# Kernel tuning notes

Measured on AMD Instinct MI355X. Metric: run time of the kernel, lower is better.

Reference implementation:

```python
import jax, jax.numpy as jnp
import numpy as np

EMBED_DIM = 2048
N_HEADS = 32
N_GROUPS = 8
HEAD_SIZE = EMBED_DIM // N_HEADS  # 64
SCALE = HEAD_SIZE ** -0.5
B, S = 2, 2048


def setup_inputs() -> dict:
    key = jax.random.key(0)
    ks = jax.random.split(key, 7)
    kv_dim = N_GROUPS * HEAD_SIZE
    x = jax.random.normal(ks[0], (B, S, EMBED_DIM), dtype=jnp.float32)
    # Linear weights stored [in, out] (y = x @ W), matching torch nn.Linear math.
    Wq = jax.random.normal(ks[1], (EMBED_DIM, EMBED_DIM), dtype=jnp.float32) * (EMBED_DIM ** -0.5)
    Wk = jax.random.normal(ks[2], (EMBED_DIM, kv_dim), dtype=jnp.float32) * (EMBED_DIM ** -0.5)
    Wv = jax.random.normal(ks[3], (EMBED_DIM, kv_dim), dtype=jnp.float32) * (EMBED_DIM ** -0.5)
    Wo = jax.random.normal(ks[4], (EMBED_DIM, EMBED_DIM), dtype=jnp.float32) * (EMBED_DIM ** -0.5)
    bo = jnp.zeros((EMBED_DIM,), dtype=jnp.float32)
    # causal boolean mask [S, S], broadcast over batch and heads
    mask = jnp.tril(jnp.ones((S, S), dtype=jnp.bool_))
    return {"x": x, "Wq": Wq, "Wk": Wk, "Wv": Wv, "Wo": Wo, "bo": bo, "mask": mask}


def reference(x, Wq, Wk, Wv, Wo, bo, mask):
    B_, S_, E = x.shape
    q = (x @ Wq).reshape(B_, S_, N_HEADS, HEAD_SIZE).transpose(0, 2, 1, 3)   # [B,H,S,D]
    k = (x @ Wk).reshape(B_, S_, N_GROUPS, HEAD_SIZE).transpose(0, 2, 1, 3)  # [B,G,S,D]
    v = (x @ Wv).reshape(B_, S_, N_GROUPS, HEAD_SIZE).transpose(0, 2, 1, 3)
    # GQA: each KV head serves H//G consecutive query heads (matches torch expand+reshape)
    rep = N_HEADS // N_GROUPS
    k = jnp.repeat(k, rep, axis=1)  # [B,H,S,D]
    v = jnp.repeat(v, rep, axis=1)
    scores = SCALE * jnp.einsum("bhqd,bhkd->bhqk", q, k)          # [B,H,S,S]
    scores = jnp.where(mask, scores, -jnp.inf)
    weights = jax.nn.softmax(scores, axis=-1)                      # dropout in eval mode (identity)
    attn = jnp.einsum("bhqk,bhkd->bhqd", weights, v)               # [B,H,S,D]
    attn = attn.transpose(0, 2, 1, 3).reshape(B_, S_, E)
    return attn @ Wo + bo
```

## Files before the change

### kernel.cpp

```cpp
#include <hip/hip_runtime.h>
#include <hip/hip_fp16.h>

#define E_DIM 2048
#define S_LEN 2048
#define NH 32
#define HD 64
#define KV_DIM 512
#define QKV_N 3072
#define M_ROWS 4096
#define QK_SCALE 0.18033688011112042f

typedef __bf16 bf16x8 __attribute__((ext_vector_type(8)));
typedef float f32x4 __attribute__((ext_vector_type(4)));

__device__ __forceinline__ void async_lds16(const __bf16* g, __bf16* l) {
    __builtin_amdgcn_global_load_lds(
        (const __attribute__((address_space(1))) void*)g,
        (__attribute__((address_space(3))) void*)l, 16, 0, 0);
}

#define BAR() asm volatile("s_barrier" ::: "memory")

__global__ void k_convert(const float* __restrict__ x, __bf16* __restrict__ xb, int n) {
    int i = (blockIdx.x * blockDim.x + threadIdx.x) * 4;
    if (i < n) {
        float4 v = *(const float4*)(x + i);
        xb[i + 0] = (__bf16)v.x;
        xb[i + 1] = (__bf16)v.y;
        xb[i + 2] = (__bf16)v.z;
        xb[i + 3] = (__bf16)v.w;
    }
}

__global__ void k_transpose_all(const float* __restrict__ Wq, const float* __restrict__ Wk,
                                const float* __restrict__ Wv, const float* __restrict__ Wo,
                                __bf16* __restrict__ WtAll, __bf16* __restrict__ WoT) {
    const int which = blockIdx.z;
    const float* W;
    __bf16* dst;
    int N;
    float scale = 1.f;
    if (which == 0)      { W = Wq; dst = WtAll;                                    N = E_DIM;  scale = QK_SCALE; }
    else if (which == 1) { W = Wk; dst = WtAll + (size_t)E_DIM * E_DIM;            N = KV_DIM; }
    else if (which == 2) { W = Wv; dst = WtAll + (size_t)(E_DIM + KV_DIM) * E_DIM; N = KV_DIM; }
    else                 { W = Wo; dst = WoT;                                      N = E_DIM;  }
    const int n0 = blockIdx.x * 32;
    if (n0 >= N) return;
    const int k0 = blockIdx.y * 32;
    __shared__ float tile[32][33];
    int tx = threadIdx.x, ty = threadIdx.y;
#pragma unroll
    for (int j = 0; j < 4; ++j)
        tile[ty + j * 8][tx] = W[(size_t)(k0 + ty + j * 8) * N + n0 + tx];
    __syncthreads();
#pragma unroll
    for (int j = 0; j < 4; ++j)
        dst[(size_t)(n0 + ty + j * 8) * E_DIM + k0 + tx] = (__bf16)(tile[tx][ty + j * 8] * scale);
}

#define STG(g, l, bb, hh, kt) do {                                                              \
    async_lds16((g) + (size_t)((hh) * 128) * K + (size_t)(kt) * 64,                             \
                (l) + (bb) * 16384 + (hh) * 8192);                                              \
    async_lds16((g) + (size_t)((hh) * 128 + 64) * K + (size_t)(kt) * 64,                        \
                (l) + (bb) * 16384 + (hh) * 8192 + 4096);                                       \
} while (0)

#define LDA_(p, mq) do {                                                                        \
    _Pragma("unroll") for (int i_ = 0; i_ < 4; ++i_) {                                          \
        const char* rp_ = pAs + (p) * 32768 + ((mq) * 128 + rA + i_ * 16) * 128;                \
        a[i_][0] = *(const bf16x8*)(rp_ + swzk0);                                               \
        a[i_][1] = *(const bf16x8*)(rp_ + swzk1);                                               \
    }                                                                                           \
} while (0)

#define LDB_(p, nq, b) do {                                                                     \
    _Pragma("unroll") for (int j_ = 0; j_ < 2; ++j_) {                                          \
        const char* rp_ = pBs + (p) * 32768 + ((nq) * 128 + rB + j_ * 16) * 128;                \
        b[j_][0] = *(const bf16x8*)(rp_ + swzk0);                                               \
        b[j_][1] = *(const bf16x8*)(rp_ + swzk1);                                               \
    }                                                                                           \
} while (0)

#define MM(mq, nq, b) do {                                                                      \
    __builtin_amdgcn_s_setprio(1);                                                              \
    _Pragma("unroll") for (int i_ = 0; i_ < 4; ++i_)                                            \
    _Pragma("unroll") for (int j_ = 0; j_ < 2; ++j_) {                                          \
        acc[mq][nq][i_][j_] = __builtin_amdgcn_mfma_f32_16x16x32_bf16(                          \
            a[i_][0], b[j_][0], acc[mq][nq][i_][j_], 0, 0, 0);                                  \
        acc[mq][nq][i_][j_] = __builtin_amdgcn_mfma_f32_16x16x32_bf16(                          \
            a[i_][1], b[j_][1], acc[mq][nq][i_][j_], 0, 0, 0);                                  \
    }                                                                                           \
    __builtin_amdgcn_s_setprio(0);                                                              \
} while (0)

#define GROUP(p, kt, S1, S2, WAITSTMT) do {                                                     \
    LDA_(p, 0);                                                                                 \
    LDB_(p, 0, b0);                                                                             \
    if (S1) STG(gA, lA, (p) ^ 1, 1, (kt) + 1);                                                  \
    BAR(); MM(0, 0, b0); BAR();                                                                 \
    LDB_(p, 1, b1);                                                                             \
    if (S2) STG(gA, lA, (p), 0, (kt) + 2);                                                      \
    BAR(); MM(0, 1, b1); BAR();                                                                 \
    LDA_(p, 1);                                                                                 \
    if (S2) STG(gB, lB, (p), 0, (kt) + 2);                                                      \
    BAR(); MM(1, 1, b1); BAR();                                                                 \
    if (S2) STG(gB, lB, (p), 1, (kt) + 2);                                                      \
    WAITSTMT;                                                                                   \
    BAR(); MM(1, 0, b0); BAR();                                                                 \
} while (0)

__global__ __launch_bounds__(512, 2)
void k_gemm8(const __bf16* __restrict__ A, const __bf16* __restrict__ Bt,
             __bf16* __restrict__ C, int M, int N, int K) {
    __shared__ __attribute__((aligned(16))) __bf16 As[2][16384];
    __shared__ __attribute__((aligned(16))) __bf16 Bs[2][16384];
    const int T = K >> 6;
    const int nbx = N >> 8;
    const int bid = blockIdx.x;
    const int swz = (bid & 7) * ((int)gridDim.x >> 3) + (bid >> 3);
    const int m0 = (swz / nbx) << 8;
    const int n0 = (swz % nbx) << 8;

    const int t = threadIdx.x;
    const int lane = t & 63, w = t >> 6;
    const int quad = lane >> 4, l16 = lane & 15;
    const int wr = w >> 2, wc = w & 3;

    const int rbase = w * 8 + (lane >> 3);
    const int cswz = ((lane & 7) ^ (lane >> 3)) * 8;
    const __bf16* gA = A + (size_t)(m0 + rbase) * K + cswz;
    const __bf16* gB = Bt + (size_t)(n0 + rbase) * K + cswz;
    __bf16* lA = &As[0][0] + w * 512;
    __bf16* lB = &Bs[0][0] + w * 512;

    const int swzk0 = ((0 + quad) ^ (l16 & 7)) * 16;
    const int swzk1 = ((4 + quad) ^ (l16 & 7)) * 16;
    const int rA = wr * 64 + l16;
    const int rB = wc * 32 + l16;
    const char* pAs = (const char*)&As[0][0];
    const char* pBs = (const char*)&Bs[0][0];

    f32x4 acc[2][2][4][2] = {};
    bf16x8 a[4][2], b0[2][2], b1[2][2];

    STG(gA, lA, 0, 0, 0); STG(gA, lA, 0, 1, 0);
    STG(gB, lB, 0, 0, 0); STG(gB, lB, 0, 1, 0);
    STG(gA, lA, 1, 0, 1);
    STG(gB, lB, 1, 0, 1); STG(gB, lB, 1, 1, 1);
    asm volatile("s_waitcnt vmcnt(6)" ::: "memory");
    BAR();

    int p = 0;
    for (int kt = 0; kt < T - 2; ++kt) {
        GROUP(p, kt, 1, 1, asm volatile("s_waitcnt vmcnt(6)" ::: "memory"));
        p ^= 1;
    }
    GROUP(p, T - 2, 1, 0, asm volatile("s_waitcnt vmcnt(0)" ::: "memory"));
    p ^= 1;
    GROUP(p, T - 1, 0, 0, (void)0);

#pragma unroll
    for (int mq = 0; mq < 2; ++mq)
#pragma unroll
        for (int nq = 0; nq < 2; ++nq)
#pragma unroll
            for (int i = 0; i < 4; ++i)
#pragma unroll
                for (int j = 0; j < 2; ++j) {
                    const int row = m0 + mq * 128 + wr * 64 + i * 16 + quad * 4;
                    const int col = n0 + nq * 128 + wc * 32 + j * 16 + l16;
#pragma unroll
                    for (int r = 0; r < 4; ++r)
                        C[(size_t)(row + r) * N + col] = (__bf16)acc[mq][nq][i][j][r];
                }
    (void)M;
}

template <int OUT_F32>
__global__ __launch_bounds__(256, 2)
void k_gemm_bt(const __bf16* __restrict__ A, const __bf16* __restrict__ Bt,
               void* __restrict__ Cout, const float* __restrict__ bias,
               int M, int N, int K) {
    __shared__ __attribute__((aligned(16))) __bf16 As2[128 * 64];
    __shared__ __attribute__((aligned(16))) __bf16 Bs2[128 * 64];
    const int t = threadIdx.x;
    const int lane = t & 63, wave = t >> 6;
    const int quad = lane >> 4, l16 = lane & 15;
    const int wr = wave >> 1, wc = wave & 1;
    const int m0 = blockIdx.y * 128, n0 = blockIdx.x * 128;

    const int srow = t >> 2;
    const int sblk = (t & 3) ^ ((t >> 3) & 3);
    const __bf16* gA0 = A + (size_t)(m0 + srow) * K + sblk * 8;
    const __bf16* gA1 = gA0 + (size_t)64 * K;
    const __bf16* gB0 = Bt + (size_t)(n0 + srow) * K + sblk * 8;
    const __bf16* gB1 = gB0 + (size_t)64 * K;

    f32x4 acc[4][4] = {};

    for (int k0 = 0; k0 < K; k0 += 64) {
#pragma unroll
        for (int ks = 0; ks < 2; ++ks) {
            async_lds16(gA0 + k0 + ks * 32, As2 + ks * 4096 + wave * 512);
            async_lds16(gA1 + k0 + ks * 32, As2 + ks * 4096 + 2048 + wave * 512);
            async_lds16(gB0 + k0 + ks * 32, Bs2 + ks * 4096 + wave * 512);
            async_lds16(gB1 + k0 + ks * 32, Bs2 + ks * 4096 + 2048 + wave * 512);
        }
        __syncthreads();
#pragma unroll
        for (int ks = 0; ks < 2; ++ks) {
            bf16x8 af[4], bfr[4];
#pragma unroll
            for (int i = 0; i < 4; ++i) {
                const int row = wr * 64 + i * 16 + l16;
                af[i] = *(const bf16x8*)((const char*)As2 + ks * 8192 + row * 64 +
                                         ((quad ^ ((row >> 1) & 3)) * 16));
            }
#pragma unroll
            for (int j = 0; j < 4; ++j) {
                const int row = wc * 64 + j * 16 + l16;
                bfr[j] = *(const bf16x8*)((const char*)Bs2 + ks * 8192 + row * 64 +
                                          ((quad ^ ((row >> 1) & 3)) * 16));
            }
#pragma unroll
            for (int i = 0; i < 4; ++i)
#pragma unroll
                for (int j = 0; j < 4; ++j)
                    acc[i][j] = __builtin_amdgcn_mfma_f32_16x16x32_bf16(af[i], bfr[j], acc[i][j], 0, 0, 0);
        }
        __syncthreads();
    }

#pragma unroll
    for (int i = 0; i < 4; ++i)
#pragma unroll
        for (int j = 0; j < 4; ++j) {
            const int row = m0 + wr * 64 + i * 16 + quad * 4;
            const int col = n0 + wc * 64 + j * 16 + l16;
#pragma unroll
            for (int r = 0; r < 4; ++r) {
                float v = acc[i][j][r];
                if (OUT_F32) ((float*)Cout)[(size_t)(row + r) * N + col] = v + bias[col];
                else ((__bf16*)Cout)[(size_t)(row + r) * N + col] = (__bf16)v;
            }
        }
}

__global__ __launch_bounds__(256, 4)
void k_attn(const __bf16* __restrict__ qkv, __half* __restrict__ partO,
            float* __restrict__ partL) {
    const int xr = (int)(gridDim.x - 1 - blockIdx.x);
    int qi, c;
    if (xr < 8)       { qi = xr;                  c = 0; }
    else if (xr < 24) { qi = 8 + ((xr - 8) >> 1); c = (xr - 8) & 1; }
    else if (xr < 48) { qi = 16 + (xr - 24) / 3;  c = (xr - 24) % 3; }
    else              { qi = 24 + ((xr - 48) >> 2); c = (xr - 48) & 3; }
    const int q0 = qi * 64;
    const int k_lo = c * 512;
    const int k_hi = min(k_lo + 512, q0 + 64);

    const int gp = blockIdx.y;
    const int g = gp >> 1;
    const int h0 = g * 4 + (gp & 1) * 2;
    const int b = blockIdx.z;
    const int t = threadIdx.x;
    const int lane = t & 63, wave = t >> 6;
    const int quad = lane >> 4, l16 = lane & 15;

    __shared__ __attribute__((aligned(16))) __bf16 Kls[128 * 64];
    __shared__ __attribute__((aligned(16))) __bf16 vT[64][136];
    __shared__ __attribute__((aligned(16))) __bf16 pT[4][512];

    const __bf16* base = qkv + (size_t)b * S_LEN * QKV_N;
    const int qrow = q0 + wave * 16 + l16;

    bf16x8 qf[2][2];
#pragma unroll
    for (int h = 0; h < 2; ++h)
#pragma unroll
        for (int s = 0; s < 2; ++s)
            qf[h][s] = *(const bf16x8*)(base + (size_t)qrow * QKV_N + (h0 + h) * HD + s * 32 + quad * 8);

    f32x4 o[2][4] = {};
    float l_st[2] = {0.f, 0.f};

    const int vkey = lane * 2, vdg = wave * 16;
    const __bf16* vsrc = base + (E_DIM + KV_DIM) + g * HD + vdg;
    const __bf16* ksrc = base + E_DIM + g * HD;

    const int klocal = lane >> 3;
    const int kdblk = (lane & 7) ^ (klocal & 7);
    const __bf16* gk_base = ksrc + (size_t)(wave * 32 + klocal) * QKV_N + kdblk * 8;
    __bf16* lk_base = Kls + wave * 2048;

    const int pswz = (l16 >> 1) & 3;
    char* prow = (char*)&pT[wave][0] + l16 * 64;

    auto qk = [&](int m, f32x4* sA, f32x4* sB) {
        __builtin_amdgcn_s_setprio(1);
#pragma unroll
        for (int kt = 0; kt < 4; ++kt) {
            const int kr = m * 64 + kt * 16 + l16;
            const char* kb_ = (const char*)Kls + kr * 128;
            bf16x8 kf0 = *(const bf16x8*)(kb_ + ((quad ^ (kr & 7)) * 16));
            bf16x8 kf1 = *(const bf16x8*)(kb_ + (((4 + quad) ^ (kr & 7)) * 16));
            f32x4 z = {};
            z = __builtin_amdgcn_mfma_f32_16x16x32_bf16(kf0, qf[0][0], z, 0, 0, 0);
            sA[kt] = __builtin_amdgcn_mfma_f32_16x16x32_bf16(kf1, qf[0][1], z, 0, 0, 0);
            f32x4 ww = {};
            ww = __builtin_amdgcn_mfma_f32_16x16x32_bf16(kf0, qf[1][0], ww, 0, 0, 0);
            sB[kt] = __builtin_amdgcn_mfma_f32_16x16x32_bf16(kf1, qf[1][1], ww, 0, 0, 0);
        }
        __builtin_amdgcn_s_setprio(0);
    };

    auto smxh = [&](int kb, int half, int h, f32x4* sc) {
        const bool diag = (kb == q0);
        float lsum = 0.f;
#pragma unroll
        for (int u = 0; u < 2; ++u) {
            const int kt = 2 * half + u;
            f32x4 pv_;
#pragma unroll
            for (int r = 0; r < 4; ++r) pv_[r] = exp2f(sc[kt][r]);
            if (diag) {
                const int kbase = kb + kt * 16 + quad * 4;
#pragma unroll
                for (int r = 0; r < 4; ++r)
                    if (kbase + r > qrow) pv_[r] = 0.f;
            }
#pragma unroll
            for (int r = 0; r < 4; ++r) lsum += pv_[r];
            __bf16 pb[4];
#pragma unroll
            for (int r = 0; r < 4; ++r) pb[r] = (__bf16)pv_[r];
            const int bi = (2 * u + (quad >> 1)) ^ pswz;
            *(uint2*)(prow + bi * 16 + (quad & 1) * 8) = *(const uint2*)pb;
        }
        l_st[h] += lsum;
    };

    auto pvh = [&](int h, const bf16x8* vf) {
        bf16x8 pf = *(const bf16x8*)(prow + ((quad ^ pswz) * 16));
        __builtin_amdgcn_s_setprio(1);
#pragma unroll
        for (int cc = 0; cc < 4; ++cc)
            o[h][cc] = __builtin_amdgcn_mfma_f32_16x16x32_bf16(vf[cc], pf, o[h][cc], 0, 0, 0);
        __builtin_amdgcn_s_setprio(0);
    };

    auto process = [&](int kb, int m, f32x4* sA, f32x4* sB) {
#pragma unroll
        for (int half = 0; half < 2; ++half) {
            bf16x8 vf[4];
            const int koff = m * 64 + half * 32;
#pragma unroll
            for (int cc = 0; cc < 4; ++cc)
                vf[cc] = *(const bf16x8*)&vT[cc * 16 + l16][koff + quad * 8];
            smxh(kb, half, 0, sA);
            pvh(0, vf);
            smxh(kb, half, 1, sB);
            pvh(1, vf);
        }
    };

    for (int kv0 = k_lo; kv0 < k_hi; kv0 += 128) {
#pragma unroll
        for (int i = 0; i < 4; ++i)
            async_lds16(gk_base + (size_t)(kv0 + i * 8) * QKV_N, lk_base + i * 512);

        const __bf16* vp = vsrc + (size_t)(kv0 + vkey) * QKV_N;
        uint4 va0 = *(const uint4*)(vp);
        uint4 va1 = *(const uint4*)(vp + 8);
        uint4 vb0 = *(const uint4*)(vp + QKV_N);
        uint4 vb1 = *(const uint4*)(vp + QKV_N + 8);

        {
            const unsigned short* a0 = (const unsigned short*)&va0;
            const unsigned short* a1 = (const unsigned short*)&va1;
            const unsigned short* b0_ = (const unsigned short*)&vb0;
            const unsigned short* b1_ = (const unsigned short*)&vb1;
#pragma unroll
            for (int j = 0; j < 8; ++j) {
                *(uint32_t*)&vT[vdg + j][vkey] = (uint32_t)a0[j] | ((uint32_t)b0_[j] << 16);
                *(uint32_t*)&vT[vdg + 8 + j][vkey] = (uint32_t)a1[j] | ((uint32_t)b1_[j] << 16);
            }
        }
        __syncthreads();

        f32x4 scA[4], scB[4];
        qk(0, scA, scB);
        process(kv0, 0, scA, scB);

        const int kb1 = kv0 + 64;
        if (kb1 < k_hi) {
            qk(1, scA, scB);
            process(kb1, 1, scA, scB);
        }
        __syncthreads();
    }

    const size_t blk = ((size_t)b * 16 + gp) * 80 + xr;
    const size_t pb = blk * (2 * 64 * 64);
#pragma unroll
    for (int h = 0; h < 2; ++h) {
        float lt = l_st[h];
        lt += __shfl_xor(lt, 16);
        lt += __shfl_xor(lt, 32);
        const float inv = 1.f / lt;
        __half* prowO = partO + pb + (size_t)(h * 64 + wave * 16 + l16) * 64 + quad * 4;
#pragma unroll
        for (int dt = 0; dt < 4; ++dt) {
            __half ob[4];
#pragma unroll
            for (int r = 0; r < 4; ++r) ob[r] = __float2half(o[h][dt][r] * inv);
            *(uint2*)(prowO + dt * 16) = *(const uint2*)ob;
        }
        if (quad == 0)
            partL[blk * 128 + h * 64 + wave * 16 + l16] = lt;
    }
}

__global__ __launch_bounds__(256, 4)
void k_combine(const __half* __restrict__ partO, const float* __restrict__ partL,
               __bf16* __restrict__ attnb) {
    const int qi = blockIdx.x, gp = blockIdx.y, b = blockIdx.z;
    const int nc = (qi >> 3) + 1;
    int x0;
    if (qi < 8) x0 = qi;
    else if (qi < 16) x0 = 8 + (qi - 8) * 2;
    else if (qi < 24) x0 = 24 + (qi - 16) * 3;
    else x0 = 48 + (qi - 24) * 4;

    const int t = threadIdx.x;
    const int row = t >> 1, half = t & 1;
    const int h = row >> 6, q = row & 63;
    const int d0 = half * 32;
    const size_t gbase = ((size_t)b * 16 + gp) * 80;

    float W = 0.f;
    float acc[32];
#pragma unroll
    for (int i = 0; i < 32; ++i) acc[i] = 0.f;
    for (int cc = 0; cc < nc; ++cc) {
        const float a = partL[(gbase + x0 + cc) * 128 + h * 64 + q];
        W += a;
        const __half* src = partO + (gbase + x0 + cc) * (2 * 64 * 64) + (size_t)(h * 64 + q) * 64 + d0;
#pragma unroll
        for (int i = 0; i < 32; i += 8) {
            uint4 u = *(const uint4*)(src + i);
            const __half* hs = (const __half*)&u;
#pragma unroll
            for (int j = 0; j < 8; ++j) acc[i + j] += a * __half2float(hs[j]);
        }
    }
    const float inv = 1.f / W;
    const int h_abs = (gp >> 1) * 4 + (gp & 1) * 2 + h;
    __bf16* dst = attnb + ((size_t)b * S_LEN + qi * 64 + q) * E_DIM + h_abs * 64 + d0;
#pragma unroll
    for (int i = 0; i < 32; i += 8) {
        __bf16 ob[8];
#pragma unroll
        for (int j = 0; j < 8; ++j) ob[j] = (__bf16)(acc[i + j] * inv);
        *(uint4*)(dst + i) = *(const uint4*)ob;
    }
}

extern "C" void kernel_launch(void* const* d_in, const int* in_sizes, int n_in,
                              void* d_out, int out_size, void* d_ws, size_t ws_size,
                              hipStream_t stream) {
    const float* x  = (const float*)d_in[0];
    const float* Wq = (const float*)d_in[1];
    const float* Wk = (const float*)d_in[2];
    const float* Wv = (const float*)d_in[3];
    const float* Wo = (const float*)d_in[4];
    const float* bo = (const float*)d_in[5];

    __bf16* xb    = (__bf16*)d_ws;
    __bf16* WtAll = xb + (size_t)M_ROWS * E_DIM;
    __bf16* WoT   = WtAll + (size_t)QKV_N * E_DIM;
    __bf16* qkv   = WoT + (size_t)E_DIM * E_DIM;
    __bf16* attnb = qkv + (size_t)M_ROWS * QKV_N;
    __half* partO = (__half*)(attnb + (size_t)M_ROWS * E_DIM);
    float* partL  = (float*)(partO + (size_t)2560 * 2 * 64 * 64);

    k_convert<<<(M_ROWS * E_DIM / 4 + 255) / 256, 256, 0, stream>>>(x, xb, M_ROWS * E_DIM);
    k_transpose_all<<<dim3(64, 64, 4), dim3(32, 8), 0, stream>>>(Wq, Wk, Wv, Wo, WtAll, WoT);

    k_gemm8<<<dim3((M_ROWS / 256) * (QKV_N / 256)), 512, 0, stream>>>(
        xb, WtAll, qkv, M_ROWS, QKV_N, E_DIM);

    k_attn<<<dim3(80, 16, 2), 256, 0, stream>>>(qkv, partO, partL);
    k_combine<<<dim3(32, 16, 2), 256, 0, stream>>>(partO, partL, attnb);

    k_gemm_bt<1><<<dim3(E_DIM / 128, M_ROWS / 128), 256, 0, stream>>>(
        attnb, WoT, d_out, bo, M_ROWS, E_DIM, E_DIM);
}
```

Before: 321.8 us.

## Widen attention query tile to 128 rows to reuse staged K/V tiles

```diff
diff --git a/kernel.cpp b/kernel.cpp
--- a/kernel.cpp
+++ b/kernel.cpp
@@ -246,18 +246,18 @@
         }
 }
 
-__global__ __launch_bounds__(256, 4)
+__global__ __launch_bounds__(256, 3)
 void k_attn(const __bf16* __restrict__ qkv, __half* __restrict__ partO,
             float* __restrict__ partL) {
     const int xr = (int)(gridDim.x - 1 - blockIdx.x);
     int qi, c;
-    if (xr < 8)       { qi = xr;                  c = 0; }
-    else if (xr < 24) { qi = 8 + ((xr - 8) >> 1); c = (xr - 8) & 1; }
-    else if (xr < 48) { qi = 16 + (xr - 24) / 3;  c = (xr - 24) % 3; }
-    else              { qi = 24 + ((xr - 48) >> 2); c = (xr - 48) & 3; }
-    const int q0 = qi * 64;
+    if (xr < 4)       { qi = xr;                   c = 0; }
+    else if (xr < 12) { qi = 4 + ((xr - 4) >> 1);  c = (xr - 4) & 1; }
+    else if (xr < 24) { qi = 8 + (xr - 12) / 3;    c = (xr - 12) % 3; }
+    else              { qi = 12 + ((xr - 24) >> 2); c = (xr - 24) & 3; }
+    const int q0 = qi * 128;
     const int k_lo = c * 512;
-    const int k_hi = min(k_lo + 512, q0 + 64);
+    const int k_hi = min(k_lo + 512, q0 + 128);
 
     const int gp = blockIdx.y;
     const int g = gp >> 1;
@@ -269,20 +269,23 @@
 
     __shared__ __attribute__((aligned(16))) __bf16 Kls[128 * 64];
     __shared__ __attribute__((aligned(16))) __bf16 vT[64][136];
-    __shared__ __attribute__((aligned(16))) __bf16 pT[4][512];
+    __shared__ __attribute__((aligned(16))) __bf16 pT[4][2][512];
 
     const __bf16* base = qkv + (size_t)b * S_LEN * QKV_N;
-    const int qrow = q0 + wave * 16 + l16;
-
-    bf16x8 qf[2][2];
-#pragma unroll
-    for (int h = 0; h < 2; ++h)
-#pragma unroll
-        for (int s = 0; s < 2; ++s)
-            qf[h][s] = *(const bf16x8*)(base + (size_t)qrow * QKV_N + (h0 + h) * HD + s * 32 + quad * 8);
-
-    f32x4 o[2][4] = {};
-    float l_st[2] = {0.f, 0.f};
+    const int qr16 = wave * 16 + l16;
+
+    bf16x8 qf[2][2][2];
+#pragma unroll
+    for (int qs = 0; qs < 2; ++qs)
+#pragma unroll
+        for (int h = 0; h < 2; ++h)
+#pragma unroll
+            for (int s = 0; s < 2; ++s)
+                qf[qs][h][s] = *(const bf16x8*)(base + (size_t)(q0 + qs * 64 + qr16) * QKV_N +
+                                                (h0 + h) * HD + s * 32 + quad * 8);
+
+    f32x4 o[2][2][4] = {};
+    float l_st[2][2] = {};
 
     const int vkey = lane * 2, vdg = wave * 16;
     const __bf16* vsrc = base + (E_DIM + KV_DIM) + g * HD + vdg;
@@ -294,9 +297,12 @@
     __bf16* lk_base = Kls + wave * 2048;
 
     const int pswz = (l16 >> 1) & 3;
-    char* prow = (char*)&pT[wave][0] + l16 * 64;
-
-    auto qk = [&](int m, f32x4* sA, f32x4* sB) {
+
+    auto micro_pass = [&](int kb, int m, int qs) {
+        const int qsub0 = q0 + qs * 64;
+        const int qrow = qsub0 + qr16;
+        const bool diag = (kb == qsub0);
+        f32x4 sA[4], sB[4];
         __builtin_amdgcn_s_setprio(1);
 #pragma unroll
         for (int kt = 0; kt < 4; ++kt) {
@@ -305,51 +311,13 @@
             bf16x8 kf0 = *(const bf16x8*)(kb_ + ((quad ^ (kr & 7)) * 16));
             bf16x8 kf1 = *(const bf16x8*)(kb_ + (((4 + quad) ^ (kr & 7)) * 16));
             f32x4 z = {};
-            z = __builtin_amdgcn_mfma_f32_16x16x32_bf16(kf0, qf[0][0], z, 0, 0, 0);
-            sA[kt] = __builtin_amdgcn_mfma_f32_16x16x32_bf16(kf1, qf[0][1], z, 0, 0, 0);
+            z = __builtin_amdgcn_mfma_f32_16x16x32_bf16(kf0, qf[qs][0][0], z, 0, 0, 0);
+            sA[kt] = __builtin_amdgcn_mfma_f32_16x16x32_bf16(kf1, qf[qs][0][1], z, 0, 0, 0);
             f32x4 ww = {};
-            ww = __builtin_amdgcn_mfma_f32_16x16x32_bf16(kf0, qf[1][0], ww, 0, 0, 0);
-            sB[kt] = __builtin_amdgcn_mfma_f32_16x16x32_bf16(kf1, qf[1][1], ww, 0, 0, 0);
+            ww = __builtin_amdgcn_mfma_f32_16x16x32_bf16(kf0, qf[qs][1][0], ww, 0, 0, 0);
+            sB[kt] = __builtin_amdgcn_mfma_f32_16x16x32_bf16(kf1, qf[qs][1][1], ww, 0, 0, 0);
         }
         __builtin_amdgcn_s_setprio(0);
-    };
-
-    auto smxh = [&](int kb, int half, int h, f32x4* sc) {
-        const bool diag = (kb == q0);
-        float lsum = 0.f;
-#pragma unroll
-        for (int u = 0; u < 2; ++u) {
-            const int kt = 2 * half + u;
-            f32x4 pv_;
-#pragma unroll
-            for (int r = 0; r < 4; ++r) pv_[r] = exp2f(sc[kt][r]);
-            if (diag) {
-                const int kbase = kb + kt * 16 + quad * 4;
-#pragma unroll
-                for (int r = 0; r < 4; ++r)
-                    if (kbase + r > qrow) pv_[r] = 0.f;
-            }
-#pragma unroll
-            for (int r = 0; r < 4; ++r) lsum += pv_[r];
-            __bf16 pb[4];
-#pragma unroll
-            for (int r = 0; r < 4; ++r) pb[r] = (__bf16)pv_[r];
-            const int bi = (2 * u + (quad >> 1)) ^ pswz;
-            *(uint2*)(prow + bi * 16 + (quad & 1) * 8) = *(const uint2*)pb;
-        }
-        l_st[h] += lsum;
-    };
-
-    auto pvh = [&](int h, const bf16x8* vf) {
-        bf16x8 pf = *(const bf16x8*)(prow + ((quad ^ pswz) * 16));
-        __builtin_amdgcn_s_setprio(1);
-#pragma unroll
-        for (int cc = 0; cc < 4; ++cc)
-            o[h][cc] = __builtin_amdgcn_mfma_f32_16x16x32_bf16(vf[cc], pf, o[h][cc], 0, 0, 0);
-        __builtin_amdgcn_s_setprio(0);
-    };
-
-    auto process = [&](int kb, int m, f32x4* sA, f32x4* sB) {
 #pragma unroll
         for (int half = 0; half < 2; ++half) {
             bf16x8 vf[4];
@@ -357,10 +325,39 @@
 #pragma unroll
             for (int cc = 0; cc < 4; ++cc)
                 vf[cc] = *(const bf16x8*)&vT[cc * 16 + l16][koff + quad * 8];
-            smxh(kb, half, 0, sA);
-            pvh(0, vf);
-            smxh(kb, half, 1, sB);
-            pvh(1, vf);
+#pragma unroll
+            for (int h = 0; h < 2; ++h) {
+                f32x4* sc = h ? sB : sA;
+                char* prow = (char*)&pT[wave][h][0] + l16 * 64;
+                float lsum = 0.f;
+#pragma unroll
+                for (int u = 0; u < 2; ++u) {
+                    const int kt = 2 * half + u;
+                    f32x4 pv_;
+#pragma unroll
+                    for (int r = 0; r < 4; ++r) pv_[r] = exp2f(sc[kt][r]);
+                    if (diag) {
+                        const int kbase = kb + kt * 16 + quad * 4;
+#pragma unroll
+                        for (int r = 0; r < 4; ++r)
+                            if (kbase + r > qrow) pv_[r] = 0.f;
+                    }
+#pragma unroll
+                    for (int r = 0; r < 4; ++r) lsum += pv_[r];
+                    __bf16 pb[4];
+#pragma unroll
+                    for (int r = 0; r < 4; ++r) pb[r] = (__bf16)pv_[r];
+                    const int bi = (2 * u + (quad >> 1)) ^ pswz;
+                    *(uint2*)(prow + bi * 16 + (quad & 1) * 8) = *(const uint2*)pb;
+                }
+                l_st[qs][h] += lsum;
+                bf16x8 pf = *(const bf16x8*)(prow + ((quad ^ pswz) * 16));
+                __builtin_amdgcn_s_setprio(1);
+#pragma unroll
+                for (int cc = 0; cc < 4; ++cc)
+                    o[qs][h][cc] = __builtin_amdgcn_mfma_f32_16x16x32_bf16(vf[cc], pf, o[qs][h][cc], 0, 0, 0);
+                __builtin_amdgcn_s_setprio(0);
+            }
         }
     };
 
@@ -388,64 +385,64 @@
         }
         __syncthreads();
 
-        f32x4 scA[4], scB[4];
-        qk(0, scA, scB);
-        process(kv0, 0, scA, scB);
-
-        const int kb1 = kv0 + 64;
-        if (kb1 < k_hi) {
-            qk(1, scA, scB);
-            process(kb1, 1, scA, scB);
+#pragma unroll
+        for (int qs = 0; qs < 2; ++qs) {
+            micro_pass(kv0, 0, qs);
+            if (kv0 < q0 + qs * 64)
+                micro_pass(kv0 + 64, 1, qs);
         }
         __syncthreads();
     }
 
-    const size_t blk = ((size_t)b * 16 + gp) * 80 + xr;
-    const size_t pb = blk * (2 * 64 * 64);
-#pragma unroll
-    for (int h = 0; h < 2; ++h) {
-        float lt = l_st[h];
-        lt += __shfl_xor(lt, 16);
-        lt += __shfl_xor(lt, 32);
-        const float inv = 1.f / lt;
-        __half* prowO = partO + pb + (size_t)(h * 64 + wave * 16 + l16) * 64 + quad * 4;
-#pragma unroll
-        for (int dt = 0; dt < 4; ++dt) {
-            __half ob[4];
-#pragma unroll
-            for (int r = 0; r < 4; ++r) ob[r] = __float2half(o[h][dt][r] * inv);
-            *(uint2*)(prowO + dt * 16) = *(const uint2*)ob;
-        }
-        if (quad == 0)
-            partL[blk * 128 + h * 64 + wave * 16 + l16] = lt;
-    }
+    const size_t blk = ((size_t)b * 16 + gp) * 40 + xr;
+    const size_t pb = blk * (size_t)(2 * 128 * 64);
+#pragma unroll
+    for (int qs = 0; qs < 2; ++qs)
+#pragma unroll
+        for (int h = 0; h < 2; ++h) {
+            float lt = l_st[qs][h];
+            lt += __shfl_xor(lt, 16);
+            lt += __shfl_xor(lt, 32);
+            const float inv = 1.f / lt;
+            __half* prowO = partO + pb + (size_t)(h * 128 + qs * 64 + qr16) * 64 + quad * 4;
+#pragma unroll
+            for (int dt = 0; dt < 4; ++dt) {
+                __half ob[4];
+#pragma unroll
+                for (int r = 0; r < 4; ++r) ob[r] = __float2half(o[qs][h][dt][r] * inv);
+                *(uint2*)(prowO + dt * 16) = *(const uint2*)ob;
+            }
+            if (quad == 0)
+                partL[blk * 256 + h * 128 + qs * 64 + qr16] = lt;
+        }
 }
 
 __global__ __launch_bounds__(256, 4)
 void k_combine(const __half* __restrict__ partO, const float* __restrict__ partL,
                __bf16* __restrict__ attnb) {
-    const int qi = blockIdx.x, gp = blockIdx.y, b = blockIdx.z;
-    const int nc = (qi >> 3) + 1;
+    const int qh = blockIdx.x, gp = blockIdx.y, b = blockIdx.z;
+    const int qi = qh >> 1, h = qh & 1;
+    const int nc = (qi >> 2) + 1;
     int x0;
-    if (qi < 8) x0 = qi;
-    else if (qi < 16) x0 = 8 + (qi - 8) * 2;
-    else if (qi < 24) x0 = 24 + (qi - 16) * 3;
-    else x0 = 48 + (qi - 24) * 4;
+    if (qi < 4) x0 = qi;
+    else if (qi < 8) x0 = 4 + (qi - 4) * 2;
+    else if (qi < 12) x0 = 12 + (qi - 8) * 3;
+    else x0 = 24 + (qi - 12) * 4;
 
     const int t = threadIdx.x;
     const int row = t >> 1, half = t & 1;
-    const int h = row >> 6, q = row & 63;
     const int d0 = half * 32;
-    const size_t gbase = ((size_t)b * 16 + gp) * 80;
+    const size_t gbase = ((size_t)b * 16 + gp) * 40;
 
     float W = 0.f;
     float acc[32];
 #pragma unroll
     for (int i = 0; i < 32; ++i) acc[i] = 0.f;
     for (int cc = 0; cc < nc; ++cc) {
-        const float a = partL[(gbase + x0 + cc) * 128 + h * 64 + q];
+        const float a = partL[(gbase + x0 + cc) * 256 + h * 128 + row];
         W += a;
-        const __half* src = partO + (gbase + x0 + cc) * (2 * 64 * 64) + (size_t)(h * 64 + q) * 64 + d0;
+        const __half* src = partO + (gbase + x0 + cc) * (size_t)(2 * 128 * 64) +
+                            (size_t)(h * 128 + row) * 64 + d0;
 #pragma unroll
         for (int i = 0; i < 32; i += 8) {
             uint4 u = *(const uint4*)(src + i);
@@ -456,7 +453,7 @@
     }
     const float inv = 1.f / W;
     const int h_abs = (gp >> 1) * 4 + (gp & 1) * 2 + h;
-    __bf16* dst = attnb + ((size_t)b * S_LEN + qi * 64 + q) * E_DIM + h_abs * 64 + d0;
+    __bf16* dst = attnb + ((size_t)b * S_LEN + qi * 128 + row) * E_DIM + h_abs * 64 + d0;
 #pragma unroll
     for (int i = 0; i < 32; i += 8) {
         __bf16 ob[8];
@@ -482,7 +479,7 @@
     __bf16* qkv   = WoT + (size_t)E_DIM * E_DIM;
     __bf16* attnb = qkv + (size_t)M_ROWS * QKV_N;
     __half* partO = (__half*)(attnb + (size_t)M_ROWS * E_DIM);
-    float* partL  = (float*)(partO + (size_t)2560 * 2 * 64 * 64);
+    float* partL  = (float*)(partO + (size_t)1280 * 2 * 128 * 64);
 
     k_convert<<<(M_ROWS * E_DIM / 4 + 255) / 256, 256, 0, stream>>>(x, xb, M_ROWS * E_DIM);
     k_transpose_all<<<dim3(64, 64, 4), dim3(32, 8), 0, stream>>>(Wq, Wk, Wv, Wo, WtAll, WoT);
@@ -490,7 +487,7 @@
     k_gemm8<<<dim3((M_ROWS / 256) * (QKV_N / 256)), 512, 0, stream>>>(
         xb, WtAll, qkv, M_ROWS, QKV_N, E_DIM);
 
-    k_attn<<<dim3(80, 16, 2), 256, 0, stream>>>(qkv, partO, partL);
+    k_attn<<<dim3(40, 16, 2), 256, 0, stream>>>(qkv, partO, partL);
     k_combine<<<dim3(32, 16, 2), 256, 0, stream>>>(partO, partL, attnb);
 
     k_gemm_bt<1><<<dim3(E_DIM / 128, M_ROWS / 128), 256, 0, stream>>>(
```

Result: slower. 398.6 us (+23.8%).
